# Performance work log

Hardware: AMD Instinct MI355X
Metric: run time of the kernel (lower is better)

The kernel has to match this reference:

```python
import jax, jax.numpy as jnp
import numpy as np
import math

EMBED_DIM = 512
NUM_HEADS = 8
NUM_LAYERS = 6
MASK_SIZE = 32
KERNEL = 3
BATCH = 16
SEQ = MASK_SIZE * MASK_SIZE
DFF = EMBED_DIM  # dim_feedforward=embed_dim in the original
LN_EPS = 1e-5


def make_window_mask(size, kernel_size):
    # Faithful port of Transformer.generate_window_mask (additive -inf mask
    # implementing a kernel_size x kernel_size window over a size x size grid).
    pad = kernel_size // 2
    cols = [-math.inf] * pad + list(range(size)) + [-math.inf] * pad
    pad_cols = [-math.inf] * len(cols)
    rows = [pad_cols] + [[i * size + v for v in cols] for i in range(size)] + [pad_cols]
    rows = [[int(v) if v >= 0 else -1 for v in row] for row in rows]
    grid = np.array(rows, dtype=np.int64)
    mask = np.full((size * size, size * size), -np.inf, dtype=np.float32)
    r = 0
    for y in range(size):
        for x in range(size):
            idx = grid[y:y + kernel_size, x:x + kernel_size].reshape(-1)
            idx = idx[idx >= 0]
            mask[r, idx] = 0.0
            r += 1
    return jnp.asarray(mask)


def setup_inputs() -> dict:
    key = jax.random.key(0)
    ks = jax.random.split(key, 14)
    D, F, L = EMBED_DIM, DFF, NUM_LAYERS
    s = 0.02
    inp = {
        "x": jax.random.normal(ks[0], (BATCH, SEQ, D), dtype=jnp.float32),
        "ln1_g": jnp.ones((L, D), jnp.float32),
        "ln1_b": jnp.zeros((L, D), jnp.float32),
        "wqkv": jax.random.normal(ks[1], (L, 3 * D, D), jnp.float32) * s,
        "bqkv": jnp.zeros((L, 3 * D), jnp.float32),
        "wo": jax.random.normal(ks[2], (L, D, D), jnp.float32) * s,
        "bo": jnp.zeros((L, D), jnp.float32),
        "ln2_g": jnp.ones((L, D), jnp.float32),
        "ln2_b": jnp.zeros((L, D), jnp.float32),
        "w1": jax.random.normal(ks[3], (L, F, D), jnp.float32) * s,
        "b1": jnp.zeros((L, F), jnp.float32),
        "w2": jax.random.normal(ks[4], (L, D, F), jnp.float32) * s,
        "b2": jnp.zeros((L, D), jnp.float32),
        "mask": make_window_mask(MASK_SIZE, KERNEL),
    }
    return inp


def _layer_norm(x, g, b):
    m = jnp.mean(x, axis=-1, keepdims=True)
    v = jnp.mean((x - m) ** 2, axis=-1, keepdims=True)
    return (x - m) / jnp.sqrt(v + LN_EPS) * g + b


def _encoder(x, mask, ln1_g, ln1_b, wqkv, bqkv, wo, bo, ln2_g, ln2_b, w1, b1, w2, b2):
    # norm_first TransformerEncoderLayer, eval mode (dropout = no-op), gelu(exact)
    H = NUM_HEADS

    def layer(h, p):
        g1, bb1, wq, bq, wo_, bo_, g2, bb2, w1_, b1_, w2_, b2_ = p
        B, S, D = h.shape
        dh = D // H
        n = _layer_norm(h, g1, bb1)
        qkv = n @ wq.T + bq                      # [B,S,3D]
        q, k, v = jnp.split(qkv, 3, axis=-1)
        q = q.reshape(B, S, H, dh)
        k = k.reshape(B, S, H, dh)
        v = v.reshape(B, S, H, dh)
        scores = jnp.einsum("bqhd,bkhd->bhqk", q, k) / math.sqrt(dh) + mask
        attn = jax.nn.softmax(scores, axis=-1)
        o = jnp.einsum("bhqk,bkhd->bqhd", attn, v).reshape(B, S, D)
        h = h + (o @ wo_.T + bo_)
        n2 = _layer_norm(h, g2, bb2)
        ff = jax.nn.gelu(n2 @ w1_.T + b1_, approximate=False) @ w2_.T + b2_
        return h + ff, None

    out, _ = jax.lax.scan(
        layer, x, (ln1_g, ln1_b, wqkv, bqkv, wo, bo, ln2_g, ln2_b, w1, b1, w2, b2)
    )
    return out


def reference(x, ln1_g, ln1_b, wqkv, bqkv, wo, bo, ln2_g, ln2_b, w1, b1, w2, b2, mask):
    return _encoder(x, mask, ln1_g, ln1_b, wqkv, bqkv, wo, bo, ln2_g, ln2_b, w1, b1, w2, b2)
```

## Files before the change

kernel.cpp:

```cpp
#include <hip/hip_runtime.h>
#include <math.h>

#define BATCH   16
#define SEQ     1024
#define DIM     512
#define NH      8
#define DHEAD   64
#define NLAYER  6
#define MROWS   (BATCH * SEQ)
#define GR      32
#define KDIM    512
#define CHUNKB  8
#define CHUNKM  (CHUNKB * SEQ)

#define ASTRIP  4
#define KSLOTS  6
#define LSTR    68

typedef __attribute__((ext_vector_type(8))) short          bf16x8;
typedef __attribute__((ext_vector_type(4))) float          f32x4;
typedef __attribute__((ext_vector_type(8))) unsigned short u16x8;

__device__ __forceinline__ unsigned short bf16rn(float f) {
    unsigned u = __float_as_uint(f);
    u += 0x7FFFu + ((u >> 16) & 1u);
    return (unsigned short)(u >> 16);
}
__device__ __forceinline__ float bf16tof(unsigned short h) {
    return __uint_as_float(((unsigned)h) << 16);
}

__device__ __forceinline__ void gload16(const void* g, void* l) {
    __builtin_amdgcn_global_load_lds(
        (const __attribute__((address_space(1))) void*)g,
        (__attribute__((address_space(3))) void*)l,
        16, 0, 0);
}

__global__ __launch_bounds__(256)
void split_kernel(const float* __restrict__ in, unsigned short* __restrict__ hi,
                  unsigned short* __restrict__ lo, int n4) {
    int i = blockIdx.x * 256 + threadIdx.x;
    if (i >= n4) return;
    float4 v = ((const float4*)in)[i];
    ushort4 h, l;
    h.x = bf16rn(v.x); l.x = bf16rn(v.x - bf16tof(h.x));
    h.y = bf16rn(v.y); l.y = bf16rn(v.y - bf16tof(h.y));
    h.z = bf16rn(v.z); l.z = bf16rn(v.z - bf16tof(h.z));
    h.w = bf16rn(v.w); l.w = bf16rn(v.w - bf16tof(h.w));
    ((ushort4*)hi)[i] = h;
    ((ushort4*)lo)[i] = l;
}

__global__ __launch_bounds__(256)
void ln_split(const float* __restrict__ x, const float* __restrict__ g,
              const float* __restrict__ b, unsigned short* __restrict__ oh,
              unsigned short* __restrict__ ol) {
    int w    = (blockIdx.x * 256 + threadIdx.x) >> 6;
    int lane = threadIdx.x & 63;
    const float* row = x + (size_t)w * DIM;
    float4 v0 = ((const float4*)row)[lane];
    float4 v1 = ((const float4*)row)[lane + 64];

    float s = v0.x + v0.y + v0.z + v0.w + v1.x + v1.y + v1.z + v1.w;
    #pragma unroll
    for (int o = 32; o; o >>= 1) s += __shfl_xor(s, o, 64);
    float mean = s * (1.0f / DIM);

    float d0x = v0.x - mean, d0y = v0.y - mean, d0z = v0.z - mean, d0w = v0.w - mean;
    float d1x = v1.x - mean, d1y = v1.y - mean, d1z = v1.z - mean, d1w = v1.w - mean;
    float vv = d0x*d0x + d0y*d0y + d0z*d0z + d0w*d0w
             + d1x*d1x + d1y*d1y + d1z*d1z + d1w*d1w;
    #pragma unroll
    for (int o = 32; o; o >>= 1) vv += __shfl_xor(vv, o, 64);
    float r = rsqrtf(vv * (1.0f / DIM) + 1e-5f);

    float4 g0 = ((const float4*)g)[lane];
    float4 g1 = ((const float4*)g)[lane + 64];
    float4 b0 = ((const float4*)b)[lane];
    float4 b1 = ((const float4*)b)[lane + 64];

    float o0x = d0x * r * g0.x + b0.x, o0y = d0y * r * g0.y + b0.y;
    float o0z = d0z * r * g0.z + b0.z, o0w = d0w * r * g0.w + b0.w;
    float o1x = d1x * r * g1.x + b1.x, o1y = d1y * r * g1.y + b1.y;
    float o1z = d1z * r * g1.z + b1.z, o1w = d1w * r * g1.w + b1.w;

    ushort4 h0, l0, h1, l1;
    h0.x = bf16rn(o0x); l0.x = bf16rn(o0x - bf16tof(h0.x));
    h0.y = bf16rn(o0y); l0.y = bf16rn(o0y - bf16tof(h0.y));
    h0.z = bf16rn(o0z); l0.z = bf16rn(o0z - bf16tof(h0.z));
    h0.w = bf16rn(o0w); l0.w = bf16rn(o0w - bf16tof(h0.w));
    h1.x = bf16rn(o1x); l1.x = bf16rn(o1x - bf16tof(h1.x));
    h1.y = bf16rn(o1y); l1.y = bf16rn(o1y - bf16tof(h1.y));
    h1.z = bf16rn(o1z); l1.z = bf16rn(o1z - bf16tof(h1.z));
    h1.w = bf16rn(o1w); l1.w = bf16rn(o1w - bf16tof(h1.w));

    ushort4* ohr = (ushort4*)(oh + (size_t)w * DIM);
    ushort4* olr = (ushort4*)(ol + (size_t)w * DIM);
    ohr[lane]      = h0;  ohr[lane + 64] = h1;
    olr[lane]      = l0;  olr[lane + 64] = l1;
}

template <int EPI>
__global__ __launch_bounds__(256, 2)
void gemm_mfma(const unsigned short* __restrict__ Ah, const unsigned short* __restrict__ Al,
               const unsigned short* __restrict__ Wh, const unsigned short* __restrict__ Wl,
               const float* __restrict__ bias,
               float* __restrict__ C,
               unsigned short* __restrict__ Oh, unsigned short* __restrict__ Ol,
               int N) {
    __shared__ __align__(16) char smem[32768];

    const int tid  = threadIdx.x;
    const int lane = tid & 63;
    const int wid  = tid >> 6;
    const int bm = blockIdx.y, bn = blockIdx.x;
    const int wm = wid >> 1, wn = wid & 1;

    const unsigned short* aptr[4];
    const unsigned short* bptr[4];
    unsigned aoff[4], boff[4];
    #pragma unroll
    for (int i = 0; i < 4; i++) {
        int s  = i * 4 + wid;
        int hl = s >> 3, f = s & 7;
        const unsigned short* ab = hl ? Al : Ah;
        const unsigned short* bb = hl ? Wl : Wh;
        aptr[i] = ab + (size_t)(bm * 128 + f * 16 + (lane & 15)) * KDIM + ((lane >> 4) * 8);
        bptr[i] = bb + (size_t)(bn * 128 + f * 16 + (lane & 15)) * KDIM + ((lane >> 4) * 8);
        aoff[i] = (unsigned)(s * 1024);
        boff[i] = (unsigned)(16384 + s * 1024);
    }

    f32x4 acc[4][4];
    #pragma unroll
    for (int mi = 0; mi < 4; mi++)
        #pragma unroll
        for (int ni = 0; ni < 4; ni++)
            acc[mi][ni] = (f32x4){0.f, 0.f, 0.f, 0.f};

    for (int kt = 0; kt < KDIM / 32; ++kt) {
        #pragma unroll
        for (int i = 0; i < 4; i++) {
            gload16(aptr[i], smem + aoff[i]);
            gload16(bptr[i], smem + boff[i]);
            aptr[i] += 32;  bptr[i] += 32;
        }
        __syncthreads();

        bf16x8 afr[2][4], bfr[2][4];
        #pragma unroll
        for (int hl = 0; hl < 2; hl++) {
            #pragma unroll
            for (int mi = 0; mi < 4; mi++)
                afr[hl][mi] = *(const bf16x8*)(smem + (hl * 8 + wm * 4 + mi) * 1024 + lane * 16);
            #pragma unroll
            for (int ni = 0; ni < 4; ni++)
                bfr[hl][ni] = *(const bf16x8*)(smem + 16384 + (hl * 8 + wn * 4 + ni) * 1024 + lane * 16);
        }
        #pragma unroll
        for (int mi = 0; mi < 4; mi++)
            #pragma unroll
            for (int ni = 0; ni < 4; ni++) {
                acc[mi][ni] = __builtin_amdgcn_mfma_f32_16x16x32_bf16(afr[0][mi], bfr[0][ni], acc[mi][ni], 0, 0, 0);
                acc[mi][ni] = __builtin_amdgcn_mfma_f32_16x16x32_bf16(afr[0][mi], bfr[1][ni], acc[mi][ni], 0, 0, 0);
                acc[mi][ni] = __builtin_amdgcn_mfma_f32_16x16x32_bf16(afr[1][mi], bfr[0][ni], acc[mi][ni], 0, 0, 0);
            }
        __syncthreads();
    }

    const int lc = lane & 15, lr = (lane >> 4) * 4;
    const int row0 = bm * 128 + wm * 64, col0 = bn * 128 + wn * 64;
    #pragma unroll
    for (int ni = 0; ni < 4; ni++) {
        int col = col0 + ni * 16 + lc;
        float bv = bias[col];
        #pragma unroll
        for (int mi = 0; mi < 4; mi++) {
            #pragma unroll
            for (int r = 0; r < 4; r++) {
                int row = row0 + mi * 16 + lr + r;
                float v = acc[mi][ni][r] + bv;
                if (EPI == 0) {
                    C[(size_t)row * N + col] = v;
                } else if (EPI == 1) {
                    C[(size_t)row * N + col] += v;
                } else {
                    float gg = 0.5f * v * (1.0f + erff(v * 0.70710678118654752440f));
                    unsigned short hh = bf16rn(gg);
                    Oh[(size_t)row * N + col] = hh;
                    Ol[(size_t)row * N + col] = bf16rn(gg - bf16tof(hh));
                }
            }
        }
    }
}

__global__ __launch_bounds__(512)
void attn_scores(const float* __restrict__ qkv, float* __restrict__ pbuf) {
    __shared__ float tile[KSLOTS * 32 * LSTR];

    const int bidx  = blockIdx.x;
    const int strip = bidx & 7;
    const int h     = (bidx >> 3) & 7;
    const int bl    = bidx >> 6;
    const int tid   = threadIdx.x;
    const int lane  = tid & 63;
    const int w     = tid >> 6;
    const int yl    = w >> 1;
    const int xh    = w & 1;
    const int dq    = lane >> 4;
    const int xl    = lane & 15;
    const int x     = xh * 16 + xl;
    const int y0    = strip * ASTRIP;

    const float* base  = qkv + (size_t)bl * SEQ * 1536;
    const float* kbase = base + 512 + h * DHEAD;

    #pragma unroll
    for (int it = 0; it < 6; it++) {
        int fi   = tid + it * 512;
        int slot = fi >> 9;
        int rem  = fi & 511;
        int nx   = rem >> 4;
        int f4   = rem & 15;
        int gy   = y0 - 1 + slot;
        float4 v = make_float4(0.f, 0.f, 0.f, 0.f);
        if (gy >= 0 && gy < GR)
            v = *(const float4*)(kbase + (size_t)(gy * GR + nx) * 1536 + f4 * 4);
        *(float4*)&tile[(slot * 32 + nx) * LSTR + f4 * 4] = v;
    }

    const int q = (y0 + yl) * GR + x;
    const float* qp = base + (size_t)q * 1536 + h * DHEAD + dq * 16;
    float4 qv[4];
    #pragma unroll
    for (int f = 0; f < 4; f++) qv[f] = ((const float4*)qp)[f];

    __syncthreads();

    float sc[9];
    #pragma unroll
    for (int i = 0; i < 9; i++) {
        const int dy = i / 3 - 1, dx = i % 3 - 1;
        const int ny = y0 + yl + dy, nx = x + dx;
        const bool vm = (ny >= 0 && ny < GR && nx >= 0 && nx < GR);
        const int nxc = min(max(nx, 0), GR - 1);
        const float* kr = &tile[((yl + dy + 1) * 32 + nxc) * LSTR + dq * 16];
        float s = 0.f;
        #pragma unroll
        for (int f = 0; f < 4; f++) {
            float4 kv = ((const float4*)kr)[f];
            s = fmaf(qv[f].x, kv.x, s);
            s = fmaf(qv[f].y, kv.y, s);
            s = fmaf(qv[f].z, kv.z, s);
            s = fmaf(qv[f].w, kv.w, s);
        }
        s += __shfl_xor(s, 16, 64);
        s += __shfl_xor(s, 32, 64);
        sc[i] = vm ? s * 0.125f : -INFINITY;
    }

    float pmax = sc[0];
    #pragma unroll
    for (int i = 1; i < 9; i++) pmax = fmaxf(pmax, sc[i]);
    float p[9], den = 0.f;
    #pragma unroll
    for (int i = 0; i < 9; i++) {
        p[i] = expf(sc[i] - pmax);
        den += p[i];
    }
    const float inv = 1.f / den;

    if (dq == 0) {
        float* pq = pbuf + ((size_t)(bl * NH + h) * 9) * SEQ + q;
        #pragma unroll
        for (int i = 0; i < 9; i++) pq[i * SEQ] = p[i] * inv;
    }
}

__global__ __launch_bounds__(256)
void attn_pv(const float* __restrict__ qkv, const float* __restrict__ pbuf,
             unsigned short* __restrict__ oh, unsigned short* __restrict__ ol,
             int b_base) {
    const int tid  = threadIdx.x;
    const int gq   = blockIdx.x * 4 + (tid >> 6);
    const int dblk = tid & 63;
    const int bl   = gq >> 10, q = gq & (SEQ - 1);
    const int y    = q >> 5,  x = q & 31;
    const int h    = dblk >> 3;

    const float* vbase = qkv + (size_t)bl * SEQ * 1536 + 1024 + dblk * 8;
    const float* pq    = pbuf + ((size_t)(bl * NH + h) * 9) * SEQ + q;

    float acc[8];
    #pragma unroll
    for (int j = 0; j < 8; j++) acc[j] = 0.f;

    #pragma unroll
    for (int i = 0; i < 9; i++) {
        const int dy  = i / 3 - 1, dx = i % 3 - 1;
        const int nyc = min(max(y + dy, 0), GR - 1);
        const int nxc = min(max(x + dx, 0), GR - 1);
        const float w = pq[i * SEQ];
        const float* vr = vbase + (size_t)(nyc * GR + nxc) * 1536;
        float4 a = *(const float4*)(vr);
        float4 b = *(const float4*)(vr + 4);
        acc[0] = fmaf(w, a.x, acc[0]); acc[1] = fmaf(w, a.y, acc[1]);
        acc[2] = fmaf(w, a.z, acc[2]); acc[3] = fmaf(w, a.w, acc[3]);
        acc[4] = fmaf(w, b.x, acc[4]); acc[5] = fmaf(w, b.y, acc[5]);
        acc[6] = fmaf(w, b.z, acc[6]); acc[7] = fmaf(w, b.w, acc[7]);
    }

    const size_t orow = ((size_t)(b_base + bl) * SEQ + q) * DIM + dblk * 8;
    u16x8 hv, lv;
    #pragma unroll
    for (int j = 0; j < 8; j++) {
        float v = acc[j];
        unsigned short hh = bf16rn(v);
        hv[j] = hh;
        lv[j] = bf16rn(v - bf16tof(hh));
    }
    *(u16x8*)(oh + orow) = hv;
    *(u16x8*)(ol + orow) = lv;
}

extern "C" void kernel_launch(void* const* d_in, const int* in_sizes, int n_in,
                              void* d_out, int out_size, void* d_ws, size_t ws_size,
                              hipStream_t stream) {
    const float* x     = (const float*)d_in[0];
    const float* ln1_g = (const float*)d_in[1];
    const float* ln1_b = (const float*)d_in[2];
    const float* wqkv  = (const float*)d_in[3];
    const float* bqkv  = (const float*)d_in[4];
    const float* wo    = (const float*)d_in[5];
    const float* bo    = (const float*)d_in[6];
    const float* ln2_g = (const float*)d_in[7];
    const float* ln2_b = (const float*)d_in[8];
    const float* w1    = (const float*)d_in[9];
    const float* b1    = (const float*)d_in[10];
    const float* w2    = (const float*)d_in[11];
    const float* b2    = (const float*)d_in[12];

    char* ws = (char*)d_ws;
    unsigned short* wqkv_h = (unsigned short*)ws;
    unsigned short* wqkv_l = wqkv_h + 4718592;
    unsigned short* wo_h   = (unsigned short*)(ws + 18874368);
    unsigned short* wo_l   = wo_h + 1572864;
    unsigned short* w1_h   = wo_h + 2 * 1572864;
    unsigned short* w1_l   = wo_h + 3 * 1572864;
    unsigned short* w2_h   = wo_h + 4 * 1572864;
    unsigned short* w2_l   = wo_h + 5 * 1572864;
    unsigned short* Ah     = (unsigned short*)(ws + 37748736);
    unsigned short* Al     = Ah + 8388608;
    float*          qkvb   = (float*)(ws + 71303168);
    unsigned short* Fh     = (unsigned short*)(ws + 71303168);
    unsigned short* Fl     = Fh + 8388608;
    float*          pbuf   = (float*)(ws + 121634816);

    float* h = (float*)d_out;

    hipMemcpyAsync(h, x, sizeof(float) * (size_t)MROWS * DIM,
                   hipMemcpyDeviceToDevice, stream);

    split_kernel<<<4608, 256, 0, stream>>>(wqkv, wqkv_h, wqkv_l, 1179648);
    split_kernel<<<1536, 256, 0, stream>>>(wo,   wo_h,   wo_l,   393216);
    split_kernel<<<1536, 256, 0, stream>>>(w1,   w1_h,   w1_l,   393216);
    split_kernel<<<1536, 256, 0, stream>>>(w2,   w2_h,   w2_l,   393216);

    const int LN_BLOCKS = MROWS / 4;
    const int SC_BLOCKS = CHUNKB * NH * (GR / ASTRIP);
    const int PV_BLOCKS = CHUNKM / 4;

    for (int l = 0; l < NLAYER; l++) {
        const unsigned short* Wqh = wqkv_h + (size_t)l * 1536 * 512;
        const unsigned short* Wql = wqkv_l + (size_t)l * 1536 * 512;
        const unsigned short* Woh = wo_h + (size_t)l * 262144;
        const unsigned short* Wol = wo_l + (size_t)l * 262144;
        const unsigned short* W1h = w1_h + (size_t)l * 262144;
        const unsigned short* W1l = w1_l + (size_t)l * 262144;
        const unsigned short* W2h = w2_h + (size_t)l * 262144;
        const unsigned short* W2l = w2_l + (size_t)l * 262144;

        ln_split<<<LN_BLOCKS, 256, 0, stream>>>(h, ln1_g + l * DIM, ln1_b + l * DIM, Ah, Al);

        for (int c = 0; c < 2; c++) {
            gemm_mfma<0><<<dim3(12, 64), 256, 0, stream>>>(
                Ah + (size_t)c * CHUNKM * DIM, Al + (size_t)c * CHUNKM * DIM,
                Wqh, Wql, bqkv + l * 1536, qkvb, nullptr, nullptr, 1536);
            attn_scores<<<SC_BLOCKS, 512, 0, stream>>>(qkvb, pbuf);
            attn_pv<<<PV_BLOCKS, 256, 0, stream>>>(qkvb, pbuf, Ah, Al, c * CHUNKB);
        }

        gemm_mfma<1><<<dim3(4, 128), 256, 0, stream>>>(
            Ah, Al, Woh, Wol, bo + l * DIM, h, nullptr, nullptr, 512);

        ln_split<<<LN_BLOCKS, 256, 0, stream>>>(h, ln2_g + l * DIM, ln2_b + l * DIM, Ah, Al);

        gemm_mfma<2><<<dim3(4, 128), 256, 0, stream>>>(
            Ah, Al, W1h, W1l, b1 + l * DIM, nullptr, Fh, Fl, 512);

        gemm_mfma<1><<<dim3(4, 128), 256, 0, stream>>>(
            Fh, Fl, W2h, W2l, b2 + l * DIM, h, nullptr, nullptr, 512);
    }
}
```

Before: 2.135 ms.

## Pre-pack weights in MFMA tile order and double-buffer GEMM LDS stages

Measured after the change: 1.893 ms. 11.3% less time.

```diff
diff --git a/kernel.cpp b/kernel.cpp
--- a/kernel.cpp
+++ b/kernel.cpp
@@ -38,18 +38,32 @@
 }
 
 __global__ __launch_bounds__(256)
-void split_kernel(const float* __restrict__ in, unsigned short* __restrict__ hi,
-                  unsigned short* __restrict__ lo, int n4) {
-    int i = blockIdx.x * 256 + threadIdx.x;
-    if (i >= n4) return;
-    float4 v = ((const float4*)in)[i];
-    ushort4 h, l;
-    h.x = bf16rn(v.x); l.x = bf16rn(v.x - bf16tof(h.x));
-    h.y = bf16rn(v.y); l.y = bf16rn(v.y - bf16tof(h.y));
-    h.z = bf16rn(v.z); l.z = bf16rn(v.z - bf16tof(h.z));
-    h.w = bf16rn(v.w); l.w = bf16rn(v.w - bf16tof(h.w));
-    ((ushort4*)hi)[i] = h;
-    ((ushort4*)lo)[i] = l;
+void pack_w(const float* __restrict__ W, unsigned short* __restrict__ out,
+            int NT, int nlu) {
+    int gid  = blockIdx.x * 256 + threadIdx.x;
+    int l    = gid / nlu;
+    if (l >= NLAYER) return;
+    int rem  = gid - l * nlu;
+    int nt   = rem >> 14;
+    int r2   = rem & 16383;
+    int kt   = (r2 >> 10) & 15;
+    int s    = (r2 >> 6) & 15;
+    int lane = r2 & 63;
+    int hl = s >> 3, f = s & 7;
+    int row = nt * 128 + f * 16 + (lane & 15);
+    int k   = kt * 32 + (lane >> 4) * 8;
+    int N   = NT * 128;
+    const float* src = W + ((size_t)l * N + row) * 512 + k;
+    float4 a = ((const float4*)src)[0];
+    float4 b = ((const float4*)src)[1];
+    float v[8] = {a.x, a.y, a.z, a.w, b.x, b.y, b.z, b.w};
+    u16x8 o;
+    #pragma unroll
+    for (int j = 0; j < 8; j++) {
+        unsigned short hh = bf16rn(v[j]);
+        o[j] = hl ? bf16rn(v[j] - bf16tof(hh)) : hh;
+    }
+    *(u16x8*)(out + (size_t)gid * 8) = o;
 }
 
 __global__ __launch_bounds__(256)
@@ -104,12 +118,12 @@
 template <int EPI>
 __global__ __launch_bounds__(256, 2)
 void gemm_mfma(const unsigned short* __restrict__ Ah, const unsigned short* __restrict__ Al,
-               const unsigned short* __restrict__ Wh, const unsigned short* __restrict__ Wl,
+               const unsigned short* __restrict__ Wpk,
                const float* __restrict__ bias,
                float* __restrict__ C,
                unsigned short* __restrict__ Oh, unsigned short* __restrict__ Ol,
                int N) {
-    __shared__ __align__(16) char smem[32768];
+    __shared__ __align__(16) char smem[65536];
 
     const int tid  = threadIdx.x;
     const int lane = tid & 63;
@@ -117,20 +131,15 @@
     const int bm = blockIdx.y, bn = blockIdx.x;
     const int wm = wid >> 1, wn = wid & 1;
 
-    const unsigned short* aptr[4];
-    const unsigned short* bptr[4];
-    unsigned aoff[4], boff[4];
+    const unsigned short* aptr0[4];
     #pragma unroll
     for (int i = 0; i < 4; i++) {
         int s  = i * 4 + wid;
         int hl = s >> 3, f = s & 7;
         const unsigned short* ab = hl ? Al : Ah;
-        const unsigned short* bb = hl ? Wl : Wh;
-        aptr[i] = ab + (size_t)(bm * 128 + f * 16 + (lane & 15)) * KDIM + ((lane >> 4) * 8);
-        bptr[i] = bb + (size_t)(bn * 128 + f * 16 + (lane & 15)) * KDIM + ((lane >> 4) * 8);
-        aoff[i] = (unsigned)(s * 1024);
-        boff[i] = (unsigned)(16384 + s * 1024);
-    }
+        aptr0[i] = ab + (size_t)(bm * 128 + f * 16 + (lane & 15)) * KDIM + ((lane >> 4) * 8);
+    }
+    const unsigned short* bbase = Wpk + (size_t)bn * 131072 + lane * 8;
 
     f32x4 acc[4][4];
     #pragma unroll
@@ -139,24 +148,26 @@
         for (int ni = 0; ni < 4; ni++)
             acc[mi][ni] = (f32x4){0.f, 0.f, 0.f, 0.f};
 
-    for (int kt = 0; kt < KDIM / 32; ++kt) {
+    auto stage = [&](int kt, int buf) {
+        char* sb = smem + buf * 32768;
         #pragma unroll
         for (int i = 0; i < 4; i++) {
-            gload16(aptr[i], smem + aoff[i]);
-            gload16(bptr[i], smem + boff[i]);
-            aptr[i] += 32;  bptr[i] += 32;
+            int s = i * 4 + wid;
+            gload16(aptr0[i] + kt * 32, sb + s * 1024);
+            gload16(bbase + ((kt * 16 + s) << 9), sb + 16384 + s * 1024);
         }
-        __syncthreads();
-
+    };
+    auto compute = [&](int buf) {
+        const char* sb = smem + buf * 32768;
         bf16x8 afr[2][4], bfr[2][4];
         #pragma unroll
         for (int hl = 0; hl < 2; hl++) {
             #pragma unroll
             for (int mi = 0; mi < 4; mi++)
-                afr[hl][mi] = *(const bf16x8*)(smem + (hl * 8 + wm * 4 + mi) * 1024 + lane * 16);
+                afr[hl][mi] = *(const bf16x8*)(sb + (hl * 8 + wm * 4 + mi) * 1024 + lane * 16);
             #pragma unroll
             for (int ni = 0; ni < 4; ni++)
-                bfr[hl][ni] = *(const bf16x8*)(smem + 16384 + (hl * 8 + wn * 4 + ni) * 1024 + lane * 16);
+                bfr[hl][ni] = *(const bf16x8*)(sb + 16384 + (hl * 8 + wn * 4 + ni) * 1024 + lane * 16);
         }
         #pragma unroll
         for (int mi = 0; mi < 4; mi++)
@@ -166,8 +177,19 @@
                 acc[mi][ni] = __builtin_amdgcn_mfma_f32_16x16x32_bf16(afr[0][mi], bfr[1][ni], acc[mi][ni], 0, 0, 0);
                 acc[mi][ni] = __builtin_amdgcn_mfma_f32_16x16x32_bf16(afr[1][mi], bfr[0][ni], acc[mi][ni], 0, 0, 0);
             }
+    };
+
+    stage(0, 0);
+    __syncthreads();
+
+    int cur = 0;
+    for (int kt = 0; kt < 15; ++kt) {
+        stage(kt + 1, cur ^ 1);
+        compute(cur);
         __syncthreads();
-    }
+        cur ^= 1;
+    }
+    compute(cur);
 
     const int lc = lane & 15, lr = (lane >> 4) * 4;
     const int row0 = bm * 128 + wm * 64, col0 = bn * 128 + wn * 64;
@@ -343,64 +365,56 @@
     const float* b2    = (const float*)d_in[12];
 
     char* ws = (char*)d_ws;
-    unsigned short* wqkv_h = (unsigned short*)ws;
-    unsigned short* wqkv_l = wqkv_h + 4718592;
-    unsigned short* wo_h   = (unsigned short*)(ws + 18874368);
-    unsigned short* wo_l   = wo_h + 1572864;
-    unsigned short* w1_h   = wo_h + 2 * 1572864;
-    unsigned short* w1_l   = wo_h + 3 * 1572864;
-    unsigned short* w2_h   = wo_h + 4 * 1572864;
-    unsigned short* w2_l   = wo_h + 5 * 1572864;
-    unsigned short* Ah     = (unsigned short*)(ws + 37748736);
-    unsigned short* Al     = Ah + 8388608;
-    float*          qkvb   = (float*)(ws + 71303168);
-    unsigned short* Fh     = (unsigned short*)(ws + 71303168);
-    unsigned short* Fl     = Fh + 8388608;
-    float*          pbuf   = (float*)(ws + 121634816);
+    unsigned short* wqkv_pk = (unsigned short*)ws;
+    unsigned short* wo_pk   = (unsigned short*)(ws + 18874368);
+    unsigned short* w1_pk   = (unsigned short*)(ws + 25165824);
+    unsigned short* w2_pk   = (unsigned short*)(ws + 31457280);
+    unsigned short* Ah      = (unsigned short*)(ws + 37748736);
+    unsigned short* Al      = Ah + 8388608;
+    float*          qkvb    = (float*)(ws + 71303168);
+    unsigned short* Fh      = (unsigned short*)(ws + 71303168);
+    unsigned short* Fl      = Fh + 8388608;
+    float*          pbuf    = (float*)(ws + 121634816);
 
     float* h = (float*)d_out;
 
     hipMemcpyAsync(h, x, sizeof(float) * (size_t)MROWS * DIM,
                    hipMemcpyDeviceToDevice, stream);
 
-    split_kernel<<<4608, 256, 0, stream>>>(wqkv, wqkv_h, wqkv_l, 1179648);
-    split_kernel<<<1536, 256, 0, stream>>>(wo,   wo_h,   wo_l,   393216);
-    split_kernel<<<1536, 256, 0, stream>>>(w1,   w1_h,   w1_l,   393216);
-    split_kernel<<<1536, 256, 0, stream>>>(w2,   w2_h,   w2_l,   393216);
+    pack_w<<<4608, 256, 0, stream>>>(wqkv, wqkv_pk, 12, 12 * 16384);
+    pack_w<<<1536, 256, 0, stream>>>(wo,   wo_pk,   4,  4 * 16384);
+    pack_w<<<1536, 256, 0, stream>>>(w1,   w1_pk,   4,  4 * 16384);
+    pack_w<<<1536, 256, 0, stream>>>(w2,   w2_pk,   4,  4 * 16384);
 
     const int LN_BLOCKS = MROWS / 4;
     const int SC_BLOCKS = CHUNKB * NH * (GR / ASTRIP);
     const int PV_BLOCKS = CHUNKM / 4;
 
     for (int l = 0; l < NLAYER; l++) {
-        const unsigned short* Wqh = wqkv_h + (size_t)l * 1536 * 512;
-        const unsigned short* Wql = wqkv_l + (size_t)l * 1536 * 512;
-        const unsigned short* Woh = wo_h + (size_t)l * 262144;
-        const unsigned short* Wol = wo_l + (size_t)l * 262144;
-        const unsigned short* W1h = w1_h + (size_t)l * 262144;
-        const unsigned short* W1l = w1_l + (size_t)l * 262144;
-        const unsigned short* W2h = w2_h + (size_t)l * 262144;
-        const unsigned short* W2l = w2_l + (size_t)l * 262144;
+        const unsigned short* Wqp = wqkv_pk + (size_t)l * 12 * 131072;
+        const unsigned short* Wop = wo_pk   + (size_t)l * 4 * 131072;
+        const unsigned short* W1p = w1_pk   + (size_t)l * 4 * 131072;
+        const unsigned short* W2p = w2_pk   + (size_t)l * 4 * 131072;
 
         ln_split<<<LN_BLOCKS, 256, 0, stream>>>(h, ln1_g + l * DIM, ln1_b + l * DIM, Ah, Al);
 
         for (int c = 0; c < 2; c++) {
             gemm_mfma<0><<<dim3(12, 64), 256, 0, stream>>>(
                 Ah + (size_t)c * CHUNKM * DIM, Al + (size_t)c * CHUNKM * DIM,
-                Wqh, Wql, bqkv + l * 1536, qkvb, nullptr, nullptr, 1536);
+                Wqp, bqkv + l * 1536, qkvb, nullptr, nullptr, 1536);
             attn_scores<<<SC_BLOCKS, 512, 0, stream>>>(qkvb, pbuf);
             attn_pv<<<PV_BLOCKS, 256, 0, stream>>>(qkvb, pbuf, Ah, Al, c * CHUNKB);
         }
 
         gemm_mfma<1><<<dim3(4, 128), 256, 0, stream>>>(
-            Ah, Al, Woh, Wol, bo + l * DIM, h, nullptr, nullptr, 512);
+            Ah, Al, Wop, bo + l * DIM, h, nullptr, nullptr, 512);
 
         ln_split<<<LN_BLOCKS, 256, 0, stream>>>(h, ln2_g + l * DIM, ln2_b + l * DIM, Ah, Al);
 
         gemm_mfma<2><<<dim3(4, 128), 256, 0, stream>>>(
-            Ah, Al, W1h, W1l, b1 + l * DIM, nullptr, Fh, Fl, 512);
+            Ah, Al, W1p, b1 + l * DIM, nullptr, Fh, Fl, 512);
 
         gemm_mfma<1><<<dim3(4, 128), 256, 0, stream>>>(
-            Fh, Fl, W2h, W2l, b2 + l * DIM, h, nullptr, nullptr, 512);
-    }
-}
+            Fh, Fl, W2p, b2 + l * DIM, h, nullptr, nullptr, 512);
+    }
+}
```
